# Optimization experiments

Hardware: AMD Instinct MI355X
Metric: run time of the kernel (lower is better)

## Reference

```python
import jax, jax.numpy as jnp
import numpy as np

STRIDE = 8
RATIOS = (0.33, 0.5, 1.0, 2.0, 3.0)
SCALES = (8,)
SEARCH = 255
SCORE = 25                      # (255-127)//8 + 1 + 8
A = len(RATIOS) * len(SCALES)   # 5 anchors per location
THR_HIGH = 0.6
THR_LOW = 0.3
POS_NUM = 16
TOTAL_NUM = 64


def _gen_anchors():
    # Replicates pysot Anchors.generate_all_anchors (corner format, flattened y,x,a)
    base = np.zeros((A, 4), dtype=np.float32)
    sz = STRIDE * STRIDE
    c = 0
    for r in RATIOS:
        ws = int(np.sqrt(sz / r)); hs = int(ws * r)
        for s in SCALES:
            w = ws * s; h = hs * s
            base[c] = [-w * 0.5, -h * 0.5, w * 0.5, h * 0.5]
            c += 1
    ori = SEARCH // 2 - (SCORE // 2) * STRIDE
    xs = ori + STRIDE * np.arange(SCORE, dtype=np.float32)
    cx, cy = np.meshgrid(xs, xs)  # row index = y, col index = x
    ctr = np.stack([cx, cy, cx, cy], -1).reshape(SCORE, SCORE, 1, 4)
    return (base.reshape(1, 1, A, 4) + ctr).reshape(-1, 4).astype(np.float32)


def setup_inputs() -> dict:
    key = jax.random.key(0)
    b, G = 128, 64
    k1, k2 = jax.random.split(key)
    xy = jax.random.uniform(k1, (b, G, 2), minval=0.0, maxval=170.0)
    wh = jax.random.uniform(k2, (b, G, 2), minval=20.0, maxval=70.0)
    gt_boxes = jnp.concatenate([xy, xy + wh], axis=-1)  # valid corner boxes in-image
    return {"gt_boxes": gt_boxes, "anchors": jnp.asarray(_gen_anchors()), "size": SCORE, "neg": 0}


def _overlaps(anchors, gt):
    aw = anchors[:, 2] - anchors[:, 0] + 1.0
    ah = anchors[:, 3] - anchors[:, 1] + 1.0
    area_a = (aw * ah)[None, :, None]
    gw = gt[..., 2] - gt[..., 0] + 1.0
    gh = gt[..., 3] - gt[..., 1] + 1.0
    area_g = (gw * gh)[:, None, :]
    ix = (jnp.minimum(anchors[None, :, None, 2], gt[:, None, :, 2])
          - jnp.maximum(anchors[None, :, None, 0], gt[:, None, :, 0]) + 1.0)
    iy = (jnp.minimum(anchors[None, :, None, 3], gt[:, None, :, 3])
          - jnp.maximum(anchors[None, :, None, 1], gt[:, None, :, 1]) + 1.0)
    inter = jnp.clip(ix, 0.0) * jnp.clip(iy, 0.0)
    return inter / (area_a + area_g - inter)


def _transform(anchors, gt):
    # anchors (N,4), gt (b,N,4) -> (b,N,4) deltas (dx,dy,dw,dh)
    aw = anchors[:, 2] - anchors[:, 0] + 1.0
    ah = anchors[:, 3] - anchors[:, 1] + 1.0
    acx = anchors[:, 0] + 0.5 * aw
    acy = anchors[:, 1] + 0.5 * ah
    gw = gt[..., 2] - gt[..., 0] + 1.0
    gh = gt[..., 3] - gt[..., 1] + 1.0
    gcx = gt[..., 0] + 0.5 * gw
    gcy = gt[..., 1] + 0.5 * gh
    dx = (gcx - acx[None]) / aw[None]
    dy = (gcy - acy[None]) / ah[None]
    dw = jnp.log(gw / aw[None])
    dh = jnp.log(gh / ah[None])
    return jnp.stack([dx, dy, dw, dh], axis=-1)


def reference(gt_boxes, anchors, size, neg):
    b = gt_boxes.shape[0]
    N = anchors.shape[0]
    ov = _overlaps(anchors, gt_boxes)          # (b,N,G) dominant intermediate
    max_ov = jnp.max(ov, axis=2)               # (b,N)
    arg = jnp.argmax(ov, axis=2)               # (b,N)
    gt_max = jnp.max(ov, axis=1)               # (b,G)

    cls = jnp.full((b, N), -1, dtype=jnp.int32)
    cls = jnp.where(max_ov >= THR_HIGH, 1, cls)
    cls = jnp.where(max_ov <= THR_LOW, 0, cls)
    gt_max = jnp.where(gt_max == 0.0, 1e-5, gt_max)
    keep = jnp.sum((ov == gt_max[:, None, :]).astype(jnp.int32), axis=2)
    cls = jnp.where(keep > 0, 1, cls)

    # Deterministic pos/neg subsampling (original uses np.random permutation;
    # we keep the first POS_NUM / TOTAL_NUM by anchor index per batch).
    pos = cls == 1
    cls = jnp.where(pos & (jnp.cumsum(pos.astype(jnp.int32), axis=1) > POS_NUM), -1, cls)
    negm = cls == 0
    cls = jnp.where(negm & (jnp.cumsum(negm.astype(jnp.int32), axis=1) > TOTAL_NUM), -1, cls)

    matched = jnp.take_along_axis(gt_boxes, arg[..., None], axis=1)  # (b,N,4)
    bt = _transform(anchors, matched)                                # (b,N,4)

    # Replicates original bug: pos_num taken from LAST batch element only.
    pos_num = jnp.sum((cls[-1] == 1).astype(jnp.int32))
    bw = jnp.where(cls == 1, 1.0 / pos_num.astype(gt_boxes.dtype), 0.0).astype(gt_boxes.dtype)

    # allowed_border is large -> all anchors inside -> _unmap is identity.
    cls_o = cls.reshape(b, size, size, A).transpose(0, 3, 1, 2)
    bt_o = bt.reshape(b, size, size, A, 4).transpose(0, 4, 3, 1, 2)
    bw_o = bw.reshape(b, size, size, A).transpose(0, 3, 1, 2)
    return cls_o, bt_o, bw_o, max_ov
```

## Files before the change

kernel.cpp:

```cpp
#include <hip/hip_runtime.h>


namespace {
constexpr int B_   = 128;
constexpr int N_   = 3125;
constexpr int G_   = 64;
constexpr int A_   = 5;
constexpr int S_   = 25;
constexpr int POSN = 16;
constexpr int TOTN = 64;

constexpr int CLS_OFF = 0;
constexpr int BT_OFF  = B_ * A_ * S_ * S_;
constexpr int BW_OFF  = BT_OFF + B_ * 4 * A_ * S_ * S_;
constexpr int MO_OFF  = BW_OFF + B_ * A_ * S_ * S_;
}

__device__ __forceinline__ float area_f(float x0, float y0, float x1, float y1) {
#pragma clang fp contract(off)
  return ((x1 - x0) + 1.0f) * ((y1 - y0) + 1.0f);
}

__device__ __forceinline__ float iou_f(float a0, float a1, float a2, float a3,
                                       float aarea, float g0, float g1,
                                       float g2, float g3, float garea) {
#pragma clang fp contract(off)
  float ix = (fminf(a2, g2) - fmaxf(a0, g0)) + 1.0f;
  float iy = (fminf(a3, g3) - fmaxf(a1, g1)) + 1.0f;
  ix = fmaxf(ix, 0.0f);
  iy = fmaxf(iy, 0.0f);
  float inter = ix * iy;
  return inter / ((aarea + garea) - inter);
}

__global__ __launch_bounds__(256) void k2_main(
    const float* __restrict__ gt,
    const float* __restrict__ anchors,
    float* __restrict__ out,
    int* __restrict__ cls0,
    int* __restrict__ pos_part) {
#pragma clang fp contract(off)
  const int b = blockIdx.y;
  const int t = threadIdx.x;
  const int n = blockIdx.x * 256 + t;

  __shared__ float s_gt[G_ * 4];
  __shared__ float s_garea[G_];
  __shared__ float s_gtmax[G_];
  __shared__ float s_ax[G_][2][A_];
  __shared__ int   s_pc;

  if (t == 0) s_pc = 0;
  s_gt[t] = gt[b * G_ * 4 + t];
  __syncthreads();

  if (t < 2 * G_) {
    const int g    = t >> 1;
    const int axis = t & 1;
    const float Glo = s_gt[g * 4 + axis];
    const float Ghi = s_gt[g * 4 + 2 + axis];
#pragma unroll
    for (int s = 0; s < A_; ++s) {
      const float HW[A_] = {52.f, 44.f, 32.f, 20.f, 16.f};
      const float HH[A_] = {16.f, 20.f, 32.f, 40.f, 48.f};
      const float H = axis ? HH[s] : HW[s];
      float mx = 0.0f;
#pragma unroll
      for (int p = 0; p < S_; ++p) {
        const float c = 31.0f + 8.0f * (float)p;
        float v = (fminf(c + H, Ghi) - fmaxf(c - H, Glo)) + 1.0f;
        mx = fmaxf(mx, fmaxf(v, 0.0f));
      }
      s_ax[g][axis][s] = mx;
    }
  }
  if (t < G_) {
    s_garea[t] =
        area_f(s_gt[t * 4 + 0], s_gt[t * 4 + 1], s_gt[t * 4 + 2], s_gt[t * 4 + 3]);
  }
  __syncthreads();

  if (t < G_) {
    const float AA[A_] = {3465.f, 3649.f, 4225.f, 3321.f, 3201.f};
    const float garea = s_garea[t];
    float m = 0.0f;
#pragma unroll
    for (int s = 0; s < A_; ++s) {
      const float inter = s_ax[t][0][s] * s_ax[t][1][s];
      const float uni = (AA[s] + garea) - inter;
      m = fmaxf(m, inter / uni);
    }
    s_gtmax[t] = (m == 0.0f) ? 1e-5f : m;
  }
  __syncthreads();

  if (n < N_) {
    const float4 aa = ((const float4*)anchors)[n];
    const float aw = (aa.z - aa.x) + 1.0f;
    const float ah = (aa.w - aa.y) + 1.0f;
    const float aarea = aw * ah;

    float best = -1.0f;
    int barg = 0;
    int keep = 0;
#pragma unroll 8
    for (int g = 0; g < G_; ++g) {
      const float4 gg = *(const float4*)&s_gt[g * 4];
      const float v = iou_f(aa.x, aa.y, aa.z, aa.w, aarea,
                            gg.x, gg.y, gg.z, gg.w, s_garea[g]);
      if (v > best) { best = v; barg = g; }
      keep |= (v == s_gtmax[g]);
    }

    int cc = -1;
    if (best >= 0.6f) cc = 1;
    if (best <= 0.3f) cc = 0;
    if (keep) cc = 1;
    cls0[b * N_ + n] = cc;
    if (b == B_ - 1 && cc == 1) atomicAdd(&s_pc, 1);

    const float m0 = s_gt[barg * 4 + 0], m1 = s_gt[barg * 4 + 1];
    const float m2 = s_gt[barg * 4 + 2], m3 = s_gt[barg * 4 + 3];
    const float gw = (m2 - m0) + 1.0f;
    const float gh = (m3 - m1) + 1.0f;
    const float acx = aa.x + 0.5f * aw;
    const float acy = aa.y + 0.5f * ah;
    const float gcx = m0 + 0.5f * gw;
    const float gcy = m1 + 0.5f * gh;
    const float dx = (gcx - acx) / aw;
    const float dy = (gcy - acy) / ah;
    const float dw = logf(gw / aw);
    const float dh = logf(gh / ah);

    const int a = n % A_;
    const int rem = n / A_;
    const int x = rem % S_;
    const int y = rem / S_;
    const int spat = y * S_ + x;

    float* __restrict__ out_bt = out + BT_OFF;
    const int btb = ((b * 4 + 0) * A_ + a) * (S_ * S_) + spat;
    out_bt[btb + 0 * A_ * S_ * S_] = dx;
    out_bt[btb + 1 * A_ * S_ * S_] = dy;
    out_bt[btb + 2 * A_ * S_ * S_] = dw;
    out_bt[btb + 3 * A_ * S_ * S_] = dh;

    out[MO_OFF + b * N_ + n] = best;
  }
  __syncthreads();
  if (t == 0 && b == B_ - 1) pos_part[blockIdx.x] = s_pc;
}

__global__ __launch_bounds__(256) void k3_caps_bw(
    float* __restrict__ out, const int* __restrict__ cls0,
    const int* __restrict__ pos_part) {
  const int b = blockIdx.x;
  const int t = threadIdx.x;
  __shared__ int s_c[N_];
  __shared__ int s_p[256];
  __shared__ int s_n[256];
  __shared__ int s_parts[16];

  if (t < 13) s_parts[t] = pos_part[t];
#pragma unroll
  for (int k = 0; k < 13; ++k) {
    const int i = k * 256 + t;
    if (i < N_) s_c[i] = cls0[b * N_ + i];
  }
  __syncthreads();

  const int n0 = t * 13;
  int cvals[13];
  int myp = 0, myn = 0;
#pragma unroll
  for (int k = 0; k < 13; ++k) {
    const int n = n0 + k;
    int cc = -1;
    if (n < N_) {
      cc = s_c[n];
      if (cc == 1) ++myp;
      else if (cc == 0) ++myn;
    }
    cvals[k] = cc;
  }
  s_p[t] = myp;
  s_n[t] = myn;
  __syncthreads();
  for (int off = 1; off < 256; off <<= 1) {
    int vp = 0, vn = 0;
    if (t >= off) { vp = s_p[t - off]; vn = s_n[t - off]; }
    __syncthreads();
    s_p[t] += vp;
    s_n[t] += vn;
    __syncthreads();
  }

  int runp = s_p[t] - myp;
  int runn = s_n[t] - myn;
#pragma unroll
  for (int k = 0; k < 13; ++k) {
    const int n = n0 + k;
    if (n >= N_) break;
    int cc = cvals[k];
    if (cc == 1) {
      if (++runp > POSN) cc = -1;
    } else if (cc == 0) {
      if (++runn > TOTN) cc = -1;
    }
    s_c[n] = __float_as_int((float)cc);
  }
  __syncthreads();

  int pc = 0;
#pragma unroll
  for (int k = 0; k < 13; ++k) pc += s_parts[k];
  const float inv = 1.0f / (float)((pc < POSN) ? pc : POSN);

#pragma unroll
  for (int k = 0; k < 13; ++k) {
    const int o = k * 256 + t;
    if (o < N_) {
      const int a  = o / 625;
      const int sp = o % 625;
      const float v = __int_as_float(s_c[sp * 5 + a]);
      out[CLS_OFF + b * N_ + o] = v;
      out[BW_OFF + b * N_ + o] = (v == 1.0f) ? inv : 0.0f;
    }
  }
}

extern "C" void kernel_launch(void* const* d_in, const int* in_sizes, int n_in,
                              void* d_out, int out_size, void* d_ws,
                              size_t ws_size, hipStream_t stream) {
  const float* gt = (const float*)d_in[0];
  const float* anchors = (const float*)d_in[1];
  float* out = (float*)d_out;
  int* pos_part = (int*)d_ws;
  int* cls0 = (int*)d_ws + 64;

  k2_main<<<dim3(13, B_), 256, 0, stream>>>(gt, anchors, out, cls0, pos_part);
  k3_caps_bw<<<B_, 256, 0, stream>>>(out, cls0, pos_part);
}
```

Measured before the change: 96.21 us.

## Compact per-block pos/neg index lists and narrow gt-max anchor search

The main kernel no longer writes a full per-anchor class array. Each block uses wave ballots to compute prefix counts and writes compact metadata: its positive/negative counts and the first 16 positive and 64 negative anchor indices. The second kernel rebuilds the class map from this metadata with a serial prefix over 13 blocks, which replaces the full 256-thread scan over 3125 entries. The per-gt best-overlap search now checks only 5 anchor centers near the box midpoint instead of all 25, and the gt data is packed into one shared array. The narrowed search assumes the maximum always lies within two strides of the center, and the positive count now comes from summed per-block counts rather than a separate atomic.

```diff
diff --git a/kernel.cpp b/kernel.cpp
--- a/kernel.cpp
+++ b/kernel.cpp
@@ -9,6 +9,8 @@
 constexpr int S_   = 25;
 constexpr int POSN = 16;
 constexpr int TOTN = 64;
+constexpr int NBLK = 13;
+constexpr int MS   = 82;
 
 constexpr int CLS_OFF = 0;
 constexpr int BT_OFF  = B_ * A_ * S_ * S_;
@@ -37,52 +39,55 @@
     const float* __restrict__ gt,
     const float* __restrict__ anchors,
     float* __restrict__ out,
-    int* __restrict__ cls0,
-    int* __restrict__ pos_part) {
+    int* __restrict__ meta) {
 #pragma clang fp contract(off)
   const int b = blockIdx.y;
   const int t = threadIdx.x;
   const int n = blockIdx.x * 256 + t;
 
-  __shared__ float s_gt[G_ * 4];
-  __shared__ float s_garea[G_];
-  __shared__ float s_gtmax[G_];
+  __shared__ float s_gtd[G_][8];
   __shared__ float s_ax[G_][2][A_];
-  __shared__ int   s_pc;
-
-  if (t == 0) s_pc = 0;
-  s_gt[t] = gt[b * G_ * 4 + t];
+  __shared__ int   s_wt[2][4];
+
+  s_gtd[t >> 2][t & 3] = gt[b * G_ * 4 + t];
   __syncthreads();
 
   if (t < 2 * G_) {
     const int g    = t >> 1;
     const int axis = t & 1;
-    const float Glo = s_gt[g * 4 + axis];
-    const float Ghi = s_gt[g * 4 + 2 + axis];
+    const float Glo = s_gtd[g][axis];
+    const float Ghi = s_gtd[g][2 + axis];
+    const float mid = (Glo + Ghi) * 0.5f;
+    const int pm = (int)rintf((mid - 31.0f) * 0.125f);
+    float cand[5];
+#pragma unroll
+    for (int d = 0; d < 5; ++d) {
+      int p = pm - 2 + d;
+      p = p < 0 ? 0 : (p > 24 ? 24 : p);
+      cand[d] = 31.0f + 8.0f * (float)p;
+    }
+    const float HW[A_] = {52.f, 44.f, 32.f, 20.f, 16.f};
+    const float HH[A_] = {16.f, 20.f, 32.f, 40.f, 48.f};
 #pragma unroll
     for (int s = 0; s < A_; ++s) {
-      const float HW[A_] = {52.f, 44.f, 32.f, 20.f, 16.f};
-      const float HH[A_] = {16.f, 20.f, 32.f, 40.f, 48.f};
       const float H = axis ? HH[s] : HW[s];
       float mx = 0.0f;
 #pragma unroll
-      for (int p = 0; p < S_; ++p) {
-        const float c = 31.0f + 8.0f * (float)p;
-        float v = (fminf(c + H, Ghi) - fmaxf(c - H, Glo)) + 1.0f;
+      for (int d = 0; d < 5; ++d) {
+        const float v = (fminf(cand[d] + H, Ghi) - fmaxf(cand[d] - H, Glo)) + 1.0f;
         mx = fmaxf(mx, fmaxf(v, 0.0f));
       }
       s_ax[g][axis][s] = mx;
     }
-  }
-  if (t < G_) {
-    s_garea[t] =
-        area_f(s_gt[t * 4 + 0], s_gt[t * 4 + 1], s_gt[t * 4 + 2], s_gt[t * 4 + 3]);
+  } else if (t < 192) {
+    const int g = t - 128;
+    s_gtd[g][4] = area_f(s_gtd[g][0], s_gtd[g][1], s_gtd[g][2], s_gtd[g][3]);
   }
   __syncthreads();
 
   if (t < G_) {
     const float AA[A_] = {3465.f, 3649.f, 4225.f, 3321.f, 3201.f};
-    const float garea = s_garea[t];
+    const float garea = s_gtd[t][4];
     float m = 0.0f;
 #pragma unroll
     for (int s = 0; s < A_; ++s) {
@@ -90,10 +95,11 @@
       const float uni = (AA[s] + garea) - inter;
       m = fmaxf(m, inter / uni);
     }
-    s_gtmax[t] = (m == 0.0f) ? 1e-5f : m;
-  }
-  __syncthreads();
-
+    s_gtd[t][5] = (m == 0.0f) ? 1e-5f : m;
+  }
+  __syncthreads();
+
+  int cc = -2;
   if (n < N_) {
     const float4 aa = ((const float4*)anchors)[n];
     const float aw = (aa.z - aa.x) + 1.0f;
@@ -105,22 +111,21 @@
     int keep = 0;
 #pragma unroll 8
     for (int g = 0; g < G_; ++g) {
-      const float4 gg = *(const float4*)&s_gt[g * 4];
+      const float4 gg = *(const float4*)&s_gtd[g][0];
+      const float2 ge = *(const float2*)&s_gtd[g][4];
       const float v = iou_f(aa.x, aa.y, aa.z, aa.w, aarea,
-                            gg.x, gg.y, gg.z, gg.w, s_garea[g]);
+                            gg.x, gg.y, gg.z, gg.w, ge.x);
       if (v > best) { best = v; barg = g; }
-      keep |= (v == s_gtmax[g]);
-    }
-
-    int cc = -1;
+      keep |= (v == ge.y);
+    }
+
+    cc = -1;
     if (best >= 0.6f) cc = 1;
     if (best <= 0.3f) cc = 0;
     if (keep) cc = 1;
-    cls0[b * N_ + n] = cc;
-    if (b == B_ - 1 && cc == 1) atomicAdd(&s_pc, 1);
-
-    const float m0 = s_gt[barg * 4 + 0], m1 = s_gt[barg * 4 + 1];
-    const float m2 = s_gt[barg * 4 + 2], m3 = s_gt[barg * 4 + 3];
+
+    const float m0 = s_gtd[barg][0], m1 = s_gtd[barg][1];
+    const float m2 = s_gtd[barg][2], m3 = s_gtd[barg][3];
     const float gw = (m2 - m0) + 1.0f;
     const float gh = (m3 - m1) + 1.0f;
     const float acx = aa.x + 0.5f * aw;
@@ -147,82 +152,104 @@
 
     out[MO_OFF + b * N_ + n] = best;
   }
-  __syncthreads();
-  if (t == 0 && b == B_ - 1) pos_part[blockIdx.x] = s_pc;
+
+  const int lane = t & 63;
+  const int wv   = t >> 6;
+  const int pflag = (cc == 1);
+  const int nflag = (cc == 0);
+  const unsigned long long bp = __ballot(pflag);
+  const unsigned long long bn = __ballot(nflag);
+  const unsigned long long ltm = (1ull << lane) - 1ull;
+  const int pp = __popcll(bp & ltm);
+  const int pn = __popcll(bn & ltm);
+  if (lane == 0) {
+    s_wt[0][wv] = __popcll(bp);
+    s_wt[1][wv] = __popcll(bn);
+  }
+  __syncthreads();
+  int wop = 0, won = 0, totp = 0, totn = 0;
+#pragma unroll
+  for (int i = 0; i < 4; ++i) {
+    const int ap = s_wt[0][i], an = s_wt[1][i];
+    if (i < wv) { wop += ap; won += an; }
+    totp += ap;
+    totn += an;
+  }
+  const int base = (b * NBLK + blockIdx.x) * MS;
+  if (pflag && (wop + pp) < POSN) meta[base + 2 + wop + pp] = n;
+  if (nflag && (won + pn) < TOTN) meta[base + 2 + POSN + won + pn] = n;
+  if (t == 0) {
+    meta[base + 0] = totp;
+    meta[base + 1] = totn;
+  }
 }
 
 __global__ __launch_bounds__(256) void k3_caps_bw(
-    float* __restrict__ out, const int* __restrict__ cls0,
-    const int* __restrict__ pos_part) {
+    float* __restrict__ out, const int* __restrict__ meta) {
   const int b = blockIdx.x;
   const int t = threadIdx.x;
-  __shared__ int s_c[N_];
-  __shared__ int s_p[256];
-  __shared__ int s_n[256];
-  __shared__ int s_parts[16];
-
-  if (t < 13) s_parts[t] = pos_part[t];
+  __shared__ int   s_m[NBLK * MS];
+  __shared__ int   s_cls[N_];
+  __shared__ int   s_ppre[NBLK];
+  __shared__ int   s_npre[NBLK];
+  __shared__ int   s_pc127[NBLK];
+  __shared__ float s_inv;
+
+#pragma unroll
+  for (int k = 0; k < 5; ++k) {
+    const int i = k * 256 + t;
+    if (i < NBLK * MS) s_m[i] = meta[b * NBLK * MS + i];
+  }
+  if (t < NBLK) s_pc127[t] = meta[((B_ - 1) * NBLK + t) * MS];
 #pragma unroll
   for (int k = 0; k < 13; ++k) {
     const int i = k * 256 + t;
-    if (i < N_) s_c[i] = cls0[b * N_ + i];
-  }
-  __syncthreads();
-
-  const int n0 = t * 13;
-  int cvals[13];
-  int myp = 0, myn = 0;
-#pragma unroll
-  for (int k = 0; k < 13; ++k) {
-    const int n = n0 + k;
-    int cc = -1;
-    if (n < N_) {
-      cc = s_c[n];
-      if (cc == 1) ++myp;
-      else if (cc == 0) ++myn;
-    }
-    cvals[k] = cc;
-  }
-  s_p[t] = myp;
-  s_n[t] = myn;
-  __syncthreads();
-  for (int off = 1; off < 256; off <<= 1) {
-    int vp = 0, vn = 0;
-    if (t >= off) { vp = s_p[t - off]; vn = s_n[t - off]; }
-    __syncthreads();
-    s_p[t] += vp;
-    s_n[t] += vn;
-    __syncthreads();
-  }
-
-  int runp = s_p[t] - myp;
-  int runn = s_n[t] - myn;
-#pragma unroll
-  for (int k = 0; k < 13; ++k) {
-    const int n = n0 + k;
-    if (n >= N_) break;
-    int cc = cvals[k];
-    if (cc == 1) {
-      if (++runp > POSN) cc = -1;
-    } else if (cc == 0) {
-      if (++runn > TOTN) cc = -1;
-    }
-    s_c[n] = __float_as_int((float)cc);
-  }
-  __syncthreads();
-
-  int pc = 0;
-#pragma unroll
-  for (int k = 0; k < 13; ++k) pc += s_parts[k];
-  const float inv = 1.0f / (float)((pc < POSN) ? pc : POSN);
-
+    if (i < N_) s_cls[i] = 0xBF800000;
+  }
+  __syncthreads();
+
+  if (t == 0) {
+    int ap = 0, an = 0, pc = 0;
+#pragma unroll
+    for (int j = 0; j < NBLK; ++j) {
+      s_ppre[j] = ap;
+      s_npre[j] = an;
+      ap += s_m[j * MS + 0];
+      an += s_m[j * MS + 1];
+      pc += s_pc127[j];
+    }
+    s_inv = 1.0f / (float)((pc < POSN) ? pc : POSN);
+  }
+  __syncthreads();
+
+  if (t < NBLK * POSN) {
+    const int j = t >> 4, i = t & 15;
+    const int c = s_m[j * MS + 0];
+    const int cv = (c < POSN) ? c : POSN;
+    if (i < cv && (s_ppre[j] + i) < POSN)
+      s_cls[s_m[j * MS + 2 + i]] = 0x3F800000;
+  }
+#pragma unroll
+  for (int k = 0; k < 4; ++k) {
+    const int idx = k * 256 + t;
+    if (idx < NBLK * TOTN) {
+      const int j = idx >> 6, i = idx & 63;
+      const int c = s_m[j * MS + 1];
+      const int cv = (c < TOTN) ? c : TOTN;
+      if (i < cv && (s_npre[j] + i) < TOTN)
+        s_cls[s_m[j * MS + 2 + POSN + i]] = 0;
+    }
+  }
+  __syncthreads();
+
+  const float inv = s_inv;
 #pragma unroll
   for (int k = 0; k < 13; ++k) {
     const int o = k * 256 + t;
     if (o < N_) {
       const int a  = o / 625;
       const int sp = o % 625;
-      const float v = __int_as_float(s_c[sp * 5 + a]);
+      const float v = __int_as_float(s_cls[sp * 5 + a]);
       out[CLS_OFF + b * N_ + o] = v;
       out[BW_OFF + b * N_ + o] = (v == 1.0f) ? inv : 0.0f;
     }
@@ -235,9 +262,8 @@
   const float* gt = (const float*)d_in[0];
   const float* anchors = (const float*)d_in[1];
   float* out = (float*)d_out;
-  int* pos_part = (int*)d_ws;
-  int* cls0 = (int*)d_ws + 64;
-
-  k2_main<<<dim3(13, B_), 256, 0, stream>>>(gt, anchors, out, cls0, pos_part);
-  k3_caps_bw<<<B_, 256, 0, stream>>>(out, cls0, pos_part);
-}
+  int* meta = (int*)d_ws;
+
+  k2_main<<<dim3(NBLK, B_), 256, 0, stream>>>(gt, anchors, out, meta);
+  k3_caps_bw<<<B_, 256, 0, stream>>>(out, meta);
+}
```

Result: faster. 92.64 us (-3.7%).
